# Kernel optimization log

Hardware: AMD Instinct MI355X
Metric: run time of the kernel (lower is better)

## Reference

```python
import jax, jax.numpy as jnp
import numpy as np

N, F, C, E = 1024, 64, 4, 32768
H = 256       # MLP hidden width
C_OUT = 4     # new edge channels produced by nn_edge


def setup_inputs() -> dict:
    key = jax.random.key(0)
    ks = jax.random.split(key, 12)
    x = jax.random.normal(ks[0], (N, F), dtype=jnp.float32)
    edge_index = jax.random.randint(ks[1], (C, 2, E), 0, N)
    edge_weight = jax.random.uniform(ks[2], (C, E), dtype=jnp.float32)
    s_n1 = 1.0 / np.sqrt(C * F)
    s_n2 = 1.0 / np.sqrt(H)
    s_e1 = 1.0 / np.sqrt(C + 2 * F)
    return {
        "x": x,
        "edge_index": edge_index,
        "edge_weight": edge_weight,
        "Wn1": jax.random.normal(ks[3], (C * F, H), dtype=jnp.float32) * s_n1,
        "bn1": jnp.zeros((H,), jnp.float32),
        "Wn2": jax.random.normal(ks[4], (H, F), dtype=jnp.float32) * s_n2,
        "bn2": jnp.zeros((F,), jnp.float32),
        "We1": jax.random.normal(ks[5], (C + 2 * F, H), dtype=jnp.float32) * s_e1,
        "be1": jnp.zeros((H,), jnp.float32),
        "We2": jax.random.normal(ks[6], (H, C_OUT), dtype=jnp.float32) * s_n2,
        "be2": jnp.zeros((C_OUT,), jnp.float32),
        "eps": jnp.zeros((), jnp.float32),
    }


def reference(x, edge_index, edge_weight, Wn1, bn1, Wn2, bn2, We1, be1, We2, be2, eps):
    # ---- MCGNN: per-channel edge-weighted scatter-add aggregation ----
    def agg_one(ei, w):
        # ei: [2,E] (row0 = source j, row1 = target i); w: [E]
        msg = x[ei[0]] * w[:, None]                       # [E,F]
        return jax.ops.segment_sum(msg, ei[1], num_segments=N)  # [N,F]

    agg = jax.vmap(agg_one)(edge_index, edge_weight)      # [C,N,F]
    out_cat = agg + (1.0 + eps) * x                       # broadcast self term
    h = out_cat.transpose(1, 0, 2).reshape(N, C * F)      # [N, C*F]
    x_next = jax.nn.relu(h @ Wn1 + bn1) @ Wn2 + bn2       # [N,F]

    # ---- EDPGNN: dense adjacency per channel + broadcast x_i/x_j ----
    def dense_adj(ei, w):
        return jnp.zeros((N, N), x.dtype).at[ei[0], ei[1]].add(w)

    a = jax.vmap(dense_adj)(edge_index, edge_weight)      # [C,N,N]
    a = a.transpose(1, 2, 0)                              # [N,N,C]
    x_i = jnp.broadcast_to(x_next[:, None, :], (N, N, F))
    x_j = jnp.broadcast_to(x_next[None, :, :], (N, N, F))
    feat = jnp.concatenate([a, x_i, x_j], axis=2).reshape(N * N, C + 2 * F)
    adj_out = (jax.nn.relu(feat @ We1 + be1) @ We2 + be2).reshape(N, N, C_OUT)
    return adj_out
```

## Files before the change

### kernel.cpp

```cpp
#include <hip/hip_runtime.h>

#define NN 1024
#define FF 64
#define CC 4
#define EE 32768
#define HH 256

#define OFF_ADENSE 0u
#define OFF_CNT    4194304u
#define OFF_OFFS   4198400u
#define OFF_CURSOR 4202512u
#define OFF_SRTS   4206608u
#define OFF_SRTW   4337680u
#define OFF_P      4468752u
#define OFF_Q      4730896u

__global__ __launch_bounds__(256)
void k_count(const int* __restrict__ ei, int* __restrict__ cnt)
{
    unsigned t = blockIdx.x * 256u + threadIdx.x;
    unsigned e = t & (EE - 1u);
    unsigned c = t >> 15;
    int dst = ei[c * 2 * EE + EE + e];
    atomicAdd(&cnt[c * NN + dst], 1);
}

__global__ __launch_bounds__(256)
void k_scan(const int* __restrict__ cnt, int* __restrict__ offs, int* __restrict__ cursor)
{
    __shared__ int wsum[4];
    const int t = threadIdx.x;
    int c[16];
    int s = 0;
    const int4* cp = (const int4*)(cnt + t * 16);
#pragma unroll
    for (int u = 0; u < 4; ++u) {
        int4 v = cp[u];
        c[u * 4 + 0] = v.x; c[u * 4 + 1] = v.y; c[u * 4 + 2] = v.z; c[u * 4 + 3] = v.w;
        s += v.x + v.y + v.z + v.w;
    }
    int incl = s;
#pragma unroll
    for (int d = 1; d < 64; d <<= 1) {
        int v = __shfl_up(incl, d, 64);
        if ((t & 63) >= d) incl += v;
    }
    const int w = t >> 6;
    if ((t & 63) == 63) wsum[w] = incl;
    __syncthreads();
    int base = incl - s;
    for (int ww = 0; ww < w; ++ww) base += wsum[ww];
    int run = base;
#pragma unroll
    for (int u = 0; u < 16; ++u) {
        offs[t * 16 + u] = run;
        cursor[t * 16 + u] = run;
        run += c[u];
    }
    if (t == 255) offs[4096] = run;
}

__global__ __launch_bounds__(256)
void k_bucket_adj(const int* __restrict__ ei, const float* __restrict__ ew,
                  int* __restrict__ cursor, int* __restrict__ srt_src,
                  float* __restrict__ srt_w, float* __restrict__ adense)
{
    unsigned t = blockIdx.x * 256u + threadIdx.x;
    unsigned e = t & (EE - 1u);
    unsigned c = t >> 15;
    int src = ei[c * 2 * EE + e];
    int dst = ei[c * 2 * EE + EE + e];
    float w = ew[c * EE + e];
    int pos = atomicAdd(&cursor[c * NN + dst], 1);
    srt_src[pos] = src;
    srt_w[pos] = w;
    atomicAdd(&adense[((size_t)src * NN + dst) * CC + c], w);
}

__global__ __launch_bounds__(1024)
void k_node(const float* __restrict__ x, const int* __restrict__ offs,
            const int* __restrict__ srt_src, const float* __restrict__ srt_w,
            const float* __restrict__ Wn1, const float* __restrict__ bn1,
            const float* __restrict__ Wn2, const float* __restrict__ bn2,
            const float* __restrict__ We1, const float* __restrict__ be1,
            const float* __restrict__ epsp,
            float* __restrict__ P, float* __restrict__ Q)
{
    __shared__ float hval[4][256];
    __shared__ float hidl[4][256];
    __shared__ float part[4][4][64];
    __shared__ float xnl[4][64];
    const int tid = threadIdx.x;
    const int n0 = blockIdx.x * 4;

    {
        const int w = tid >> 6, lane = tid & 63;
        const int c = w & 3, nn = w >> 2;
        const int g = c * NN + (n0 + nn);
        const int beg = offs[g], end = offs[g + 1];
        float acc = 0.f;
        for (int k = beg; k < end; ++k)
            acc += x[srt_src[k] * FF + lane] * srt_w[k];
        const float ope = 1.0f + epsp[0];
        hval[nn][c * 64 + lane] = acc + ope * x[(n0 + nn) * FF + lane];
    }
    __syncthreads();

    {
        const int nn = tid >> 8, h = tid & 255;
        float acc = bn1[h];
#pragma unroll 8
        for (int k = 0; k < 256; ++k)
            acc += hval[nn][k] * Wn1[k * 256 + h];
        hidl[nn][h] = fmaxf(acc, 0.f);
    }
    __syncthreads();

    {
        const int kq = tid >> 8, nn = (tid >> 6) & 3, f = tid & 63;
        float p = 0.f;
#pragma unroll 8
        for (int k = kq * 64; k < kq * 64 + 64; ++k)
            p += hidl[nn][k] * Wn2[k * 64 + f];
        part[kq][nn][f] = p;
    }
    __syncthreads();
    if (tid < 256) {
        const int nn = tid >> 6, f = tid & 63;
        xnl[nn][f] = bn2[f] + part[0][nn][f] + part[1][nn][f]
                             + part[2][nn][f] + part[3][nn][f];
    }
    __syncthreads();

    {
        const int r = tid >> 8, h = tid & 255;
        float p = be1[h], q = 0.f;
#pragma unroll 8
        for (int f = 0; f < 64; ++f) {
            float xv = xnl[r][f];
            p += xv * We1[(4 + f) * 256 + h];
            q += xv * We1[(68 + f) * 256 + h];
        }
        P[(n0 + r) * 256 + h] = p;
        Q[(n0 + r) * 256 + h] = q;
    }
}

__global__ __launch_bounds__(256, 4)
void k_edge_mlp(const float* __restrict__ P, const float* __restrict__ Q,
                const float* __restrict__ adense, const float* __restrict__ We1,
                const float* __restrict__ We2, const float* __restrict__ be2,
                float* __restrict__ out)
{
    __shared__ float4 Pl[32 * 16];
    __shared__ float4 Ql[32 * 16];

    const int tid = threadIdx.x;
    const int tx = tid & 15, ty = tid >> 4;
    const int iBase = blockIdx.y * 32, jBase = blockIdx.x * 32;
    const int psw = ty & 7;
    const int qsw = tx & 7;

    float4 a[2][2], acc[2][2];
#pragma unroll
    for (int ii = 0; ii < 2; ++ii)
#pragma unroll
        for (int jj = 0; jj < 2; ++jj) {
            a[ii][jj] = *(const float4*)(adense +
                ((size_t)(iBase + ty * 2 + ii) * NN + (jBase + tx * 2 + jj)) * 4);
            acc[ii][jj] = make_float4(0.f, 0.f, 0.f, 0.f);
        }

    for (int hc = 0; hc < 4; ++hc) {
        __syncthreads();
#pragma unroll
        for (int u = 0; u < 2; ++u) {
            int idx = tid + u * 256;
            int row = idx >> 4, q = idx & 15;
            int ph = q ^ ((row >> 1) & 7);
            Pl[row * 16 + ph] = *(const float4*)(P + (iBase + row) * 256 + hc * 64 + q * 4);
            Ql[row * 16 + ph] = *(const float4*)(Q + (jBase + row) * 256 + hc * 64 + q * 4);
        }
        __syncthreads();

        for (int q = 0; q < 16; ++q) {
            float4 w1[4], w2[4];
#pragma unroll
            for (int c = 0; c < 4; ++c)
                w1[c] = *(const float4*)(We1 + c * 256 + hc * 64 + q * 4);
#pragma unroll
            for (int k = 0; k < 4; ++k)
                w2[k] = *(const float4*)(We2 + (hc * 64 + q * 4 + k) * 4);

            float4 p[2], qv[2];
#pragma unroll
            for (int r = 0; r < 2; ++r) p[r]  = Pl[(ty * 2 + r) * 16 + (q ^ psw)];
#pragma unroll
            for (int r = 0; r < 2; ++r) qv[r] = Ql[(tx * 2 + r) * 16 + (q ^ qsw)];

#pragma unroll
            for (int ii = 0; ii < 2; ++ii) {
#pragma unroll
                for (int jj = 0; jj < 2; ++jj) {
                    const float4 av = a[ii][jj];
                    float s0 = av.x * w1[0].x + av.y * w1[1].x + av.z * w1[2].x + av.w * w1[3].x;
                    float s1 = av.x * w1[0].y + av.y * w1[1].y + av.z * w1[2].y + av.w * w1[3].y;
                    float s2 = av.x * w1[0].z + av.y * w1[1].z + av.z * w1[2].z + av.w * w1[3].z;
                    float s3 = av.x * w1[0].w + av.y * w1[1].w + av.z * w1[2].w + av.w * w1[3].w;
                    float v0 = fmaxf(p[ii].x + qv[jj].x + s0, 0.f);
                    float v1 = fmaxf(p[ii].y + qv[jj].y + s1, 0.f);
                    float v2 = fmaxf(p[ii].z + qv[jj].z + s2, 0.f);
                    float v3 = fmaxf(p[ii].w + qv[jj].w + s3, 0.f);
                    acc[ii][jj].x += v0 * w2[0].x + v1 * w2[1].x + v2 * w2[2].x + v3 * w2[3].x;
                    acc[ii][jj].y += v0 * w2[0].y + v1 * w2[1].y + v2 * w2[2].y + v3 * w2[3].y;
                    acc[ii][jj].z += v0 * w2[0].z + v1 * w2[1].z + v2 * w2[2].z + v3 * w2[3].z;
                    acc[ii][jj].w += v0 * w2[0].w + v1 * w2[1].w + v2 * w2[2].w + v3 * w2[3].w;
                }
            }
        }
    }

    const float4 b2 = *(const float4*)be2;
#pragma unroll
    for (int ii = 0; ii < 2; ++ii)
#pragma unroll
        for (int jj = 0; jj < 2; ++jj) {
            float4 o = acc[ii][jj];
            o.x += b2.x; o.y += b2.y; o.z += b2.z; o.w += b2.w;
            *(float4*)(out + ((size_t)(iBase + ty * 2 + ii) * NN + (jBase + tx * 2 + jj)) * 4) = o;
        }
}

extern "C" void kernel_launch(void* const* d_in, const int* in_sizes, int n_in,
                              void* d_out, int out_size, void* d_ws, size_t ws_size,
                              hipStream_t stream)
{
    (void)in_sizes; (void)n_in; (void)out_size; (void)ws_size;
    const float* x   = (const float*)d_in[0];
    const int*   ei  = (const int*)d_in[1];
    const float* ew  = (const float*)d_in[2];
    const float* Wn1 = (const float*)d_in[3];
    const float* bn1 = (const float*)d_in[4];
    const float* Wn2 = (const float*)d_in[5];
    const float* bn2 = (const float*)d_in[6];
    const float* We1 = (const float*)d_in[7];
    const float* be1 = (const float*)d_in[8];
    const float* We2 = (const float*)d_in[9];
    const float* be2 = (const float*)d_in[10];
    const float* eps = (const float*)d_in[11];
    float* out = (float*)d_out;

    float* ws = (float*)d_ws;
    float* adense = ws + OFF_ADENSE;
    int*   cnt    = (int*)(ws + OFF_CNT);
    int*   offs   = (int*)(ws + OFF_OFFS);
    int*   cursor = (int*)(ws + OFF_CURSOR);
    int*   srts   = (int*)(ws + OFF_SRTS);
    float* srtw   = ws + OFF_SRTW;
    float* Pb     = ws + OFF_P;
    float* Qb     = ws + OFF_Q;

    hipMemsetAsync(d_ws, 0, (size_t)(4194304 + 4096) * sizeof(float), stream);

    k_count     <<<(CC * EE) / 256, 256, 0, stream>>>(ei, cnt);
    k_scan      <<<1, 256, 0, stream>>>(cnt, offs, cursor);
    k_bucket_adj<<<(CC * EE) / 256, 256, 0, stream>>>(ei, ew, cursor, srts, srtw, adense);
    k_node      <<<NN / 4, 1024, 0, stream>>>(x, offs, srts, srtw,
                                              Wn1, bn1, Wn2, bn2, We1, be1, eps, Pb, Qb);

    dim3 g(NN / 32, NN / 32);
    k_edge_mlp<<<g, 256, 0, stream>>>(Pb, Qb, adense, We1, We2, be2, out);
}
```

Baseline: 235.7 us.

## Split edge MLP into dense no-adjacency pass plus sparse fix-up over nonzero pairs

```diff
diff --git a/kernel.cpp b/kernel.cpp
--- a/kernel.cpp
+++ b/kernel.cpp
@@ -6,14 +6,19 @@
 #define EE 32768
 #define HH 256
 
+typedef float f32x4 __attribute__((ext_vector_type(4)));
+
 #define OFF_ADENSE 0u
 #define OFF_CNT    4194304u
-#define OFF_OFFS   4198400u
-#define OFF_CURSOR 4202512u
-#define OFF_SRTS   4206608u
-#define OFF_SRTW   4337680u
-#define OFF_P      4468752u
-#define OFF_Q      4730896u
+#define OFF_MASK   4198400u
+#define OFF_NPAIRS 4231168u
+#define OFF_OFFS   4231172u
+#define OFF_CURSOR 4235272u
+#define OFF_SRTS   4239368u
+#define OFF_SRTW   4370440u
+#define OFF_P      4501512u
+#define OFF_Q      4763656u
+#define OFF_PLIST  5025800u
 
 __global__ __launch_bounds__(256)
 void k_count(const int* __restrict__ ei, int* __restrict__ cnt)
@@ -63,7 +68,9 @@
 __global__ __launch_bounds__(256)
 void k_bucket_adj(const int* __restrict__ ei, const float* __restrict__ ew,
                   int* __restrict__ cursor, int* __restrict__ srt_src,
-                  float* __restrict__ srt_w, float* __restrict__ adense)
+                  float* __restrict__ srt_w, float* __restrict__ adense,
+                  unsigned* __restrict__ mask, int* __restrict__ plist,
+                  int* __restrict__ npairs)
 {
     unsigned t = blockIdx.x * 256u + threadIdx.x;
     unsigned e = t & (EE - 1u);
@@ -74,7 +81,14 @@
     int pos = atomicAdd(&cursor[c * NN + dst], 1);
     srt_src[pos] = src;
     srt_w[pos] = w;
-    atomicAdd(&adense[((size_t)src * NN + dst) * CC + c], w);
+    unsigned pair = (unsigned)src * NN + (unsigned)dst;
+    atomicAdd(&adense[(size_t)pair * CC + c], w);
+    unsigned bit = 1u << (pair & 31u);
+    unsigned old = atomicOr(&mask[pair >> 5], bit);
+    if (!(old & bit)) {
+        int q = atomicAdd(npairs, 1);
+        plist[q] = (int)pair;
+    }
 }
 
 __global__ __launch_bounds__(1024)
@@ -146,30 +160,27 @@
     }
 }
 
-__global__ __launch_bounds__(256, 4)
-void k_edge_mlp(const float* __restrict__ P, const float* __restrict__ Q,
-                const float* __restrict__ adense, const float* __restrict__ We1,
-                const float* __restrict__ We2, const float* __restrict__ be2,
-                float* __restrict__ out)
+__global__ __launch_bounds__(256, 2)
+void k_edge_base(const float* __restrict__ P, const float* __restrict__ Q,
+                 const float* __restrict__ We2, const float* __restrict__ be2,
+                 float* __restrict__ out)
 {
     __shared__ float4 Pl[32 * 16];
-    __shared__ float4 Ql[32 * 16];
+    __shared__ float4 Ql[64 * 16];
 
     const int tid = threadIdx.x;
     const int tx = tid & 15, ty = tid >> 4;
-    const int iBase = blockIdx.y * 32, jBase = blockIdx.x * 32;
+    const int iBase = blockIdx.y * 32, jBase = blockIdx.x * 64;
     const int psw = ty & 7;
     const int qsw = tx & 7;
 
-    float4 a[2][2], acc[2][2];
+    const float4 b2 = *(const float4*)be2;
+    float4 acc[2][4];
 #pragma unroll
     for (int ii = 0; ii < 2; ++ii)
 #pragma unroll
-        for (int jj = 0; jj < 2; ++jj) {
-            a[ii][jj] = *(const float4*)(adense +
-                ((size_t)(iBase + ty * 2 + ii) * NN + (jBase + tx * 2 + jj)) * 4);
-            acc[ii][jj] = make_float4(0.f, 0.f, 0.f, 0.f);
-        }
+        for (int jj = 0; jj < 4; ++jj)
+            acc[ii][jj] = b2;
 
     for (int hc = 0; hc < 4; ++hc) {
         __syncthreads();
@@ -177,40 +188,39 @@
         for (int u = 0; u < 2; ++u) {
             int idx = tid + u * 256;
             int row = idx >> 4, q = idx & 15;
-            int ph = q ^ ((row >> 1) & 7);
-            Pl[row * 16 + ph] = *(const float4*)(P + (iBase + row) * 256 + hc * 64 + q * 4);
-            Ql[row * 16 + ph] = *(const float4*)(Q + (jBase + row) * 256 + hc * 64 + q * 4);
+            Pl[row * 16 + (q ^ ((row >> 1) & 7))] =
+                *(const float4*)(P + (iBase + row) * 256 + hc * 64 + q * 4);
+        }
+#pragma unroll
+        for (int u = 0; u < 4; ++u) {
+            int idx = tid + u * 256;
+            int row = idx >> 4, q = idx & 15;
+            Ql[row * 16 + (q ^ ((row >> 2) & 7))] =
+                *(const float4*)(Q + (jBase + row) * 256 + hc * 64 + q * 4);
         }
         __syncthreads();
 
+#pragma unroll
         for (int q = 0; q < 16; ++q) {
-            float4 w1[4], w2[4];
-#pragma unroll
-            for (int c = 0; c < 4; ++c)
-                w1[c] = *(const float4*)(We1 + c * 256 + hc * 64 + q * 4);
+            float4 w2[4];
 #pragma unroll
             for (int k = 0; k < 4; ++k)
                 w2[k] = *(const float4*)(We2 + (hc * 64 + q * 4 + k) * 4);
 
-            float4 p[2], qv[2];
+            float4 p[2], qv[4];
 #pragma unroll
             for (int r = 0; r < 2; ++r) p[r]  = Pl[(ty * 2 + r) * 16 + (q ^ psw)];
 #pragma unroll
-            for (int r = 0; r < 2; ++r) qv[r] = Ql[(tx * 2 + r) * 16 + (q ^ qsw)];
+            for (int r = 0; r < 4; ++r) qv[r] = Ql[(tx * 4 + r) * 16 + (q ^ qsw)];
 
 #pragma unroll
             for (int ii = 0; ii < 2; ++ii) {
 #pragma unroll
-                for (int jj = 0; jj < 2; ++jj) {
-                    const float4 av = a[ii][jj];
-                    float s0 = av.x * w1[0].x + av.y * w1[1].x + av.z * w1[2].x + av.w * w1[3].x;
-                    float s1 = av.x * w1[0].y + av.y * w1[1].y + av.z * w1[2].y + av.w * w1[3].y;
-                    float s2 = av.x * w1[0].z + av.y * w1[1].z + av.z * w1[2].z + av.w * w1[3].z;
-                    float s3 = av.x * w1[0].w + av.y * w1[1].w + av.z * w1[2].w + av.w * w1[3].w;
-                    float v0 = fmaxf(p[ii].x + qv[jj].x + s0, 0.f);
-                    float v1 = fmaxf(p[ii].y + qv[jj].y + s1, 0.f);
-                    float v2 = fmaxf(p[ii].z + qv[jj].z + s2, 0.f);
-                    float v3 = fmaxf(p[ii].w + qv[jj].w + s3, 0.f);
+                for (int jj = 0; jj < 4; ++jj) {
+                    float v0 = fmaxf(p[ii].x + qv[jj].x, 0.f);
+                    float v1 = fmaxf(p[ii].y + qv[jj].y, 0.f);
+                    float v2 = fmaxf(p[ii].z + qv[jj].z, 0.f);
+                    float v3 = fmaxf(p[ii].w + qv[jj].w, 0.f);
                     acc[ii][jj].x += v0 * w2[0].x + v1 * w2[1].x + v2 * w2[2].x + v3 * w2[3].x;
                     acc[ii][jj].y += v0 * w2[0].y + v1 * w2[1].y + v2 * w2[2].y + v3 * w2[3].y;
                     acc[ii][jj].z += v0 * w2[0].z + v1 * w2[1].z + v2 * w2[2].z + v3 * w2[3].z;
@@ -220,15 +230,54 @@
         }
     }
 
+#pragma unroll
+    for (int ii = 0; ii < 2; ++ii)
+#pragma unroll
+        for (int jj = 0; jj < 4; ++jj) {
+            float* dst = out + ((size_t)(iBase + ty * 2 + ii) * NN + (jBase + tx * 4 + jj)) * 4;
+            f32x4 o = { acc[ii][jj].x, acc[ii][jj].y, acc[ii][jj].z, acc[ii][jj].w };
+            __builtin_nontemporal_store(o, (f32x4*)dst);
+        }
+}
+
+__global__ __launch_bounds__(256)
+void k_edge_fix(const float* __restrict__ P, const float* __restrict__ Q,
+                const float* __restrict__ adense, const float* __restrict__ We1,
+                const float* __restrict__ We2, const float* __restrict__ be2,
+                const int* __restrict__ plist, const int* __restrict__ npairs,
+                float* __restrict__ out)
+{
+    const int lane = threadIdx.x & 63;
+    const int wid = (blockIdx.x << 2) | (threadIdx.x >> 6);
+    const int nw = gridDim.x << 2;
+    const int n = npairs[0];
     const float4 b2 = *(const float4*)be2;
-#pragma unroll
-    for (int ii = 0; ii < 2; ++ii)
-#pragma unroll
-        for (int jj = 0; jj < 2; ++jj) {
-            float4 o = acc[ii][jj];
-            o.x += b2.x; o.y += b2.y; o.z += b2.z; o.w += b2.w;
-            *(float4*)(out + ((size_t)(iBase + ty * 2 + ii) * NN + (jBase + tx * 2 + jj)) * 4) = o;
-        }
+
+    for (int pidx = wid; pidx < n; pidx += nw) {
+        const int pair = plist[pidx];
+        const int i = pair >> 10, j = pair & (NN - 1);
+        const float4 a = *(const float4*)(adense + (size_t)pair * 4);
+        float o0 = 0.f, o1 = 0.f, o2 = 0.f, o3 = 0.f;
+#pragma unroll
+        for (int u = 0; u < 4; ++u) {
+            const int h = u * 64 + lane;
+            float s = a.x * We1[0 * 256 + h] + a.y * We1[1 * 256 + h]
+                    + a.z * We1[2 * 256 + h] + a.w * We1[3 * 256 + h];
+            float v = fmaxf(P[i * 256 + h] + Q[j * 256 + h] + s, 0.f);
+            const float4 w2 = *(const float4*)(We2 + h * 4);
+            o0 += v * w2.x; o1 += v * w2.y; o2 += v * w2.z; o3 += v * w2.w;
+        }
+#pragma unroll
+        for (int d = 32; d > 0; d >>= 1) {
+            o0 += __shfl_down(o0, d, 64);
+            o1 += __shfl_down(o1, d, 64);
+            o2 += __shfl_down(o2, d, 64);
+            o3 += __shfl_down(o3, d, 64);
+        }
+        if (lane == 0)
+            *(float4*)(out + (size_t)pair * 4) =
+                make_float4(o0 + b2.x, o1 + b2.y, o2 + b2.z, o3 + b2.w);
+    }
 }
 
 extern "C" void kernel_launch(void* const* d_in, const int* in_sizes, int n_in,
@@ -250,24 +299,30 @@
     const float* eps = (const float*)d_in[11];
     float* out = (float*)d_out;
 
-    float* ws = (float*)d_ws;
-    float* adense = ws + OFF_ADENSE;
-    int*   cnt    = (int*)(ws + OFF_CNT);
-    int*   offs   = (int*)(ws + OFF_OFFS);
-    int*   cursor = (int*)(ws + OFF_CURSOR);
-    int*   srts   = (int*)(ws + OFF_SRTS);
-    float* srtw   = ws + OFF_SRTW;
-    float* Pb     = ws + OFF_P;
-    float* Qb     = ws + OFF_Q;
-
-    hipMemsetAsync(d_ws, 0, (size_t)(4194304 + 4096) * sizeof(float), stream);
+    float*    ws     = (float*)d_ws;
+    float*    adense = ws + OFF_ADENSE;
+    int*      cnt    = (int*)(ws + OFF_CNT);
+    unsigned* mask   = (unsigned*)(ws + OFF_MASK);
+    int*      npair  = (int*)(ws + OFF_NPAIRS);
+    int*      offs   = (int*)(ws + OFF_OFFS);
+    int*      cursor = (int*)(ws + OFF_CURSOR);
+    int*      srts   = (int*)(ws + OFF_SRTS);
+    float*    srtw   = ws + OFF_SRTW;
+    float*    Pb     = ws + OFF_P;
+    float*    Qb     = ws + OFF_Q;
+    int*      plist  = (int*)(ws + OFF_PLIST);
+
+    (void)hipMemsetAsync(d_ws, 0, (size_t)4231172 * sizeof(float), stream);
 
     k_count     <<<(CC * EE) / 256, 256, 0, stream>>>(ei, cnt);
     k_scan      <<<1, 256, 0, stream>>>(cnt, offs, cursor);
-    k_bucket_adj<<<(CC * EE) / 256, 256, 0, stream>>>(ei, ew, cursor, srts, srtw, adense);
+    k_bucket_adj<<<(CC * EE) / 256, 256, 0, stream>>>(ei, ew, cursor, srts, srtw,
+                                                      adense, mask, plist, npair);
     k_node      <<<NN / 4, 1024, 0, stream>>>(x, offs, srts, srtw,
                                               Wn1, bn1, Wn2, bn2, We1, be1, eps, Pb, Qb);
 
-    dim3 g(NN / 32, NN / 32);
-    k_edge_mlp<<<g, 256, 0, stream>>>(Pb, Qb, adense, We1, We2, be2, out);
-}
+    dim3 gb(NN / 64, NN / 32);
+    k_edge_base<<<gb, 256, 0, stream>>>(Pb, Qb, We2, be2, out);
+    k_edge_fix <<<2048, 256, 0, stream>>>(Pb, Qb, adense, We1, We2, be2,
+                                          plist, npair, out);
+}
```

Measured after the change: 513.1 us. 2.18x slower.
